# Kernel optimization log

Hardware: AMD Instinct MI355X
Metric: run time of the kernel (lower is better)

The kernel has to match this reference:

```python
import jax, jax.numpy as jnp
import numpy as np

B, S, F = 4, 8192, 32
D, H, L = 512, 8, 4
FD = 128
WIN = 256
CF = 4
MAXSEQ = 8192
HD = D // H
NEG = -1e9


def _ln(x, g, b, eps=1e-5):
    m = jnp.mean(x, -1, keepdims=True)
    v = jnp.var(x, -1, keepdims=True)
    return (x - m) * jax.lax.rsqrt(v + eps) * g + b


def setup_inputs() -> dict:
    key = jax.random.key(0)
    ks = iter(jax.random.split(key, 64))
    def rn(shape, s=0.02):
        return jax.random.normal(next(ks), shape, dtype=jnp.float32) * s
    return dict(
        x=jax.random.normal(next(ks), (B, S, F), dtype=jnp.float32),
        timestamps=jax.random.randint(next(ks), (B, S), 0, MAXSEQ),
        W_feat=rn((F, FD)), b_feat=jnp.zeros((FD,), jnp.float32),
        emb_temp=rn((MAXSEQ, FD)),
        W_emb=rn((2 * FD, D)), b_emb=jnp.zeros((D,), jnp.float32),
        Wq=rn((L, D, D)), bq=jnp.zeros((L, D), jnp.float32),
        Wk=rn((L, D, D)), bk=jnp.zeros((L, D), jnp.float32),
        Wv=rn((L, D, D)), bv=jnp.zeros((L, D), jnp.float32),
        Wo=rn((L, D, D)), bo=jnp.zeros((L, D), jnp.float32),
        Wg=rn((L, 2 * D, D)), bg=jnp.zeros((L, D), jnp.float32),
        Wu=rn((L, 2 * D, D)), bu=jnp.zeros((L, D), jnp.float32),
        ln_g=jnp.ones((L, D), jnp.float32), ln_b=jnp.zeros((L, D), jnp.float32),
        conv_w=rn((D, D, CF)), conv_b=jnp.zeros((D,), jnp.float32),
        cn_g=jnp.ones((D,), jnp.float32), cn_b=jnp.zeros((D,), jnp.float32),
        on_g=jnp.ones((D,), jnp.float32), on_b=jnp.zeros((D,), jnp.float32),
        W_out=rn((D, F)), b_out=jnp.zeros((F,), jnp.float32),
    )


def _sparse_attn(h, wq, bq, wk, bk, wv, bv, wo, bo):
    # sliding-window attention: query block b ([b*W,(b+1)*W)) attends keys in
    # [max(0,(b-1)*W), (b+1)*W) with plain softmax (no intra-window causal mask)
    bsz, slen, _ = h.shape
    nb = slen // WIN
    def proj(wm, bm):
        return (h @ wm + bm).reshape(bsz, nb, WIN, H, HD)
    q, k, v = proj(wq, bq), proj(wk, bk), proj(wv, bv)
    def with_prev(t):
        prev = jnp.concatenate([jnp.zeros_like(t[:, :1]), t[:, :-1]], axis=1)
        return jnp.concatenate([prev, t], axis=2)  # [B, nb, 2W, H, HD]
    kk, vv = with_prev(k), with_prev(v)
    scores = jnp.einsum('bnqhd,bnkhd->bnhqk', q, kk) / float(np.sqrt(HD))
    blk = jnp.arange(nb)[:, None]
    kidx = jnp.arange(2 * WIN)[None, :]
    neg = jnp.where((blk == 0) & (kidx < WIN), NEG, 0.0).astype(scores.dtype)
    att = jax.nn.softmax(scores + neg[None, :, None, None, :], axis=-1)
    out = jnp.einsum('bnhqk,bnkhd->bnqhd', att, vv).reshape(bsz, slen, D)
    return out @ wo + bo


def reference(x, timestamps, W_feat, b_feat, emb_temp, W_emb, b_emb,
              Wq, bq, Wk, bk, Wv, bv, Wo, bo, Wg, bg, Wu, bu,
              ln_g, ln_b, conv_w, conv_b, cn_g, cn_b, on_g, on_b, W_out, b_out):
    fe = x @ W_feat + b_feat                       # [B,S,FD]
    te = emb_temp[timestamps]                      # [B,S,FD]
    h = jnp.concatenate([fe, te], axis=-1) @ W_emb + b_emb  # [B,S,D]
    mem0 = jnp.zeros_like(h)

    def layer(carry, p):
        hh, mem = carry
        wq, bq_, wk, bk_, wv, bv_, wo, bo_, wg, bg_, wu, bu_, g, bta = p
        a = _sparse_attn(hh, wq, bq_, wk, bk_, wv, bv_, wo, bo_)
        comb = jnp.concatenate([a, mem], axis=-1)
        gate = jax.nn.sigmoid(comb @ wg + bg_)
        upd = comb @ wu + bu_
        new_mem = gate * upd + (1.0 - gate) * mem
        out = _ln(a + new_mem, g, bta)
        return (out, new_mem), None

    (h, _), _ = jax.lax.scan(
        layer, (h, mem0),
        (Wq, bq, Wk, bk, Wv, bv, Wo, bo, Wg, bg, Wu, bu, ln_g, ln_b))

    # temporal compression: Conv1d with kernel=stride=CF -> block reshape + einsum
    xr = h.reshape(h.shape[0], -1, CF, D)          # [B, S/CF, CF, D]
    c = jnp.einsum('btjc,ocj->bto', xr, conv_w) + conv_b
    c = _ln(c, cn_g, cn_b)
    o = _ln(c, on_g, on_b)
    return o @ W_out + b_out                       # [B, S/CF, F]
```

## Files before the change

kernel.cpp:

```cpp
#include <hip/hip_runtime.h>

#define BATCH   4
#define SEQ     8192
#define NTOK    32768
#define FF      32
#define FDIM    128
#define DD      512
#define HEADS   8
#define HDIM    64
#define WINSZ   256
#define NBLK    32
#define LAYERS  4

typedef unsigned short u16;
typedef __attribute__((ext_vector_type(8))) short bf16x8;
typedef __attribute__((ext_vector_type(4))) float f32x4;

__device__ __forceinline__ float u2f(u16 u) {
  return __uint_as_float(((unsigned int)u) << 16);
}
__device__ __forceinline__ u16 f2u(float f) {
  return (u16)((__float_as_uint(f) + 0x8000u) >> 16);
}
__device__ __forceinline__ unsigned int pk2(float a, float b) {
  return ((__float_as_uint(a) + 0x8000u) >> 16) |
         ((__float_as_uint(b) + 0x8000u) & 0xffff0000u);
}
__device__ __forceinline__ void ld8(const u16* __restrict__ p, float* o) {
  ushort4 q0 = *(const ushort4*)p;
  ushort4 q1 = *(const ushort4*)(p + 4);
  o[0]=u2f(q0.x); o[1]=u2f(q0.y); o[2]=u2f(q0.z); o[3]=u2f(q0.w);
  o[4]=u2f(q1.x); o[5]=u2f(q1.y); o[6]=u2f(q1.z); o[7]=u2f(q1.w);
}
__device__ __forceinline__ void st8(u16* __restrict__ p, const float* v) {
  uint4 o;
  o.x = pk2(v[0], v[1]); o.y = pk2(v[2], v[3]);
  o.z = pk2(v[4], v[5]); o.w = pk2(v[6], v[7]);
  *(uint4*)p = o;
}
__device__ __forceinline__ void gl_lds16(const u16* g, u16* l) {
  __builtin_amdgcn_global_load_lds(
      (const __attribute__((address_space(1))) void*)g,
      (__attribute__((address_space(3))) void*)l, 16, 0, 0);
}

__global__ __launch_bounds__(128) void embed_kernel(
    const float* __restrict__ x, const int* __restrict__ ts,
    const float* __restrict__ W_feat, const float* __restrict__ b_feat,
    const float* __restrict__ emb, u16* __restrict__ cat)
{
  const int t = blockIdx.x;
  const int j = threadIdx.x;
  __shared__ float xs[FF];
  if (j < FF) xs[j] = x[(size_t)t*FF + j];
  __syncthreads();
  float fe = b_feat[j];
  #pragma unroll
  for (int f = 0; f < FF; ++f) fe += xs[f] * W_feat[f*FDIM + j];
  cat[(size_t)t*256 + j] = f2u(fe);
  const int tv = ts[t];
  cat[(size_t)t*256 + 128 + j] = f2u(emb[(size_t)tv*FDIM + j]);
}

__global__ __launch_bounds__(256) void transpose_w(
    const float* __restrict__ src, u16* __restrict__ dst, int K)
{
  __shared__ u16 t[32][34];
  const int bk = blockIdx.x*32, bn = blockIdx.y*32;
  const int c = threadIdx.x & 31, r8 = threadIdx.x >> 5;
  #pragma unroll
  for (int rr = 0; rr < 32; rr += 8)
    t[rr + r8][c] = f2u(src[(size_t)(bk + rr + r8)*512 + bn + c]);
  __syncthreads();
  #pragma unroll
  for (int rr = 0; rr < 32; rr += 8)
    dst[(size_t)(bn + rr + r8)*K + bk + c] = t[c][rr + r8];
}

#define WQO 0
#define WKO 262144
#define WVO 524288
#define WOO 786432
#define WGO 1048576
#define WUO 1572864

__global__ __launch_bounds__(256) void convert_layer(
    const float* __restrict__ Wq, const float* __restrict__ Wk,
    const float* __restrict__ Wv, const float* __restrict__ Wo,
    const float* __restrict__ Wg, const float* __restrict__ Wu,
    u16* __restrict__ out)
{
  __shared__ u16 t[32][34];
  const int z = blockIdx.z;
  const int K = (z < 4) ? 512 : 1024;
  const int bk = blockIdx.x*32;
  if (bk >= K) return;
  const int bn = blockIdx.y*32;
  const float* src = (z==0)?Wq:(z==1)?Wk:(z==2)?Wv:(z==3)?Wo:(z==4)?Wg:Wu;
  u16* dst = out + ((z<4) ? (size_t)z*262144 : (size_t)1048576 + (size_t)(z-4)*524288);
  const int c = threadIdx.x & 31, r8 = threadIdx.x >> 5;
  #pragma unroll
  for (int rr = 0; rr < 32; rr += 8)
    t[rr + r8][c] = f2u(src[(size_t)(bk + rr + r8)*512 + bn + c]);
  __syncthreads();
  #pragma unroll
  for (int rr = 0; rr < 32; rr += 8)
    dst[(size_t)(bn + rr + r8)*K + bk + c] = t[c][rr + r8];
}

__global__ __launch_bounds__(256) void repack_conv(
    const float* __restrict__ cw, u16* __restrict__ dst)
{
  const int t = blockIdx.x*256 + threadIdx.x;
  const int o  = t >> 11;
  const int kk = t & 2047;
  const int j  = kk >> 9;
  const int ch = kk & 511;
  dst[t] = f2u(cw[(size_t)o*2048 + ch*4 + j]);
}

template<int MODE>
__global__ __launch_bounds__(512) void mfma_gemm(
    const u16* __restrict__ A1, const u16* __restrict__ A2, int K1, int K,
    const u16* __restrict__ Bt,
    const float* __restrict__ b0, const float* __restrict__ b1,
    const float* __restrict__ b2,
    u16* __restrict__ C0, u16* __restrict__ C1, u16* __restrict__ C2)
{
  __shared__ u16 Al[128*32];
  __shared__ u16 Bl[256*32];
  const int tid  = threadIdx.x;
  const int lane = tid & 63;
  const int wave = tid >> 6;
  const int wm = (wave & 1) * 64;
  const int wn = (wave >> 1) * 64;
  const int bid = blockIdx.x + gridDim.x * blockIdx.y;
  const int xcd = bid & 7;
  const int jj  = bid >> 3;
  const int nx  = jj % gridDim.x;
  const int my  = (jj / gridDim.x) * 8 + xcd;
  const int m0 = my * 128;
  const int n0 = nx * 256;
  const int cl = lane & 15, quad = lane >> 4;
  const int arow = tid >> 2;
  const int ak   = (tid & 3) * 8;
  u16* Adst  = Al + wave*512;
  u16* Bdst0 = Bl + wave*512;
  u16* Bdst1 = Bl + 4096 + wave*512;
  const int K2 = K - K1;

  f32x4 acc[4][4];
  #pragma unroll
  for (int i = 0; i < 4; ++i)
    #pragma unroll
    for (int j = 0; j < 4; ++j)
      acc[i][j] = (f32x4){0.f, 0.f, 0.f, 0.f};

  for (int k0 = 0; k0 < K; k0 += 32) {
    const int kc = k0 + ak;
    const u16* a = (kc < K1) ? A1 + (size_t)(m0 + arow)*K1 + kc
                             : A2 + (size_t)(m0 + arow)*K2 + (kc - K1);
    gl_lds16(a, Adst);
    gl_lds16(Bt + (size_t)(n0 + arow)*K + kc,       Bdst0);
    gl_lds16(Bt + (size_t)(n0 + 128 + arow)*K + kc, Bdst1);
    __syncthreads();
    bf16x8 af[4], bfr[4];
    #pragma unroll
    for (int i = 0; i < 4; ++i) {
      af[i]  = *(const bf16x8*)(Al + (wm + i*16 + cl)*32 + quad*8);
      bfr[i] = *(const bf16x8*)(Bl + (wn + i*16 + cl)*32 + quad*8);
    }
    #pragma unroll
    for (int i = 0; i < 4; ++i)
      #pragma unroll
      for (int j = 0; j < 4; ++j)
        acc[i][j] = __builtin_amdgcn_mfma_f32_16x16x32_bf16(
            af[i], bfr[j], acc[i][j], 0, 0, 0);
    __syncthreads();
  }
  const int rq = quad * 4;
  const int colbase = n0 + wn;
  const int seg = colbase >> 9;
  const float* bias = (MODE == 0) ? b0 : (seg == 0 ? b0 : (seg == 1 ? b1 : b2));
  u16* dstR = (seg == 0) ? C0 : C1;
  #pragma unroll
  for (int j = 0; j < 4; ++j) {
    const int lc = (colbase & 511) + j*16 + cl;
    const float bb = bias[lc];
    #pragma unroll
    for (int i = 0; i < 4; ++i) {
      const int rbase = m0 + wm + i*16 + rq;
      float v[4];
      #pragma unroll
      for (int r = 0; r < 4; ++r) {
        float t = acc[i][j][r] + bb;
        if (MODE == 2 && seg == 0) t = 1.0f / (1.0f + __expf(-t));
        v[r] = t;
      }
      if (MODE == 1 && seg == 2) {
        uint2 o2;
        o2.x = pk2(v[0], v[1]); o2.y = pk2(v[2], v[3]);
        *(uint2*)(C2 + (size_t)lc*NTOK + rbase) = o2;
      } else {
        #pragma unroll
        for (int r = 0; r < 4; ++r)
          dstR[(size_t)(rbase + r)*DD + lc] = f2u(v[r]);
      }
    }
  }
}

#define EXPSC 0.18033688f
__global__ __launch_bounds__(256) void attn_kernel(
    const u16* __restrict__ q, const u16* __restrict__ k,
    const u16* __restrict__ vt, u16* __restrict__ ctx)
{
  __shared__ u16 Ks[128*72];
  __shared__ u16 Vl[64*136];
  const int bid  = blockIdx.x;
  const int head = bid & 7;
  const int n    = (bid >> 3) & 31;
  const int b    = bid >> 8;
  const int tid  = threadIdx.x;
  const int lane = tid & 63;
  const int wave = tid >> 6;
  const int cl   = lane & 15;
  const int quad = lane >> 4;
  const int qtok0 = b*SEQ + n*WINSZ + wave*64;
  const bool hi2 = (lane >= 32);
  const int srcA = cl + ((quad & 1) << 5);
  const int srcB = srcA + 16;

  bf16x8 qf[4][2];
  #pragma unroll
  for (int jf = 0; jf < 4; ++jf)
    #pragma unroll
    for (int kh = 0; kh < 2; ++kh)
      qf[jf][kh] = *(const bf16x8*)(q + (size_t)(qtok0 + jf*16 + cl)*DD
                                      + head*HDIM + kh*32 + quad*8);

  f32x4 oacc[4][4];
  #pragma unroll
  for (int i = 0; i < 4; ++i)
    #pragma unroll
    for (int j = 0; j < 4; ++j)
      oacc[i][j] = (f32x4){0.f, 0.f, 0.f, 0.f};
  float lrun[4] = {0.f, 0.f, 0.f, 0.f};

  const int r0 = (n == 0) ? WINSZ : 0;
  const int base_tok = b*SEQ + (n - 1)*WINSZ;
  const int ksr = tid >> 1;
  const int ksc = (tid & 1) * 32;
  const int vsr = tid >> 2;
  const int vsc = (tid & 3) * 32;

  for (int c0 = r0; c0 < 2*WINSZ; c0 += 128) {
    {
      const u16* ksrc = k + (size_t)(base_tok + c0 + ksr)*DD + head*HDIM + ksc;
      uint4* kd = (uint4*)(Ks + ksr*72 + ksc);
      kd[0] = ((const uint4*)ksrc)[0];
      kd[1] = ((const uint4*)ksrc)[1];
      kd[2] = ((const uint4*)ksrc)[2];
      kd[3] = ((const uint4*)ksrc)[3];
      const u16* vsrc = vt + (size_t)(head*HDIM + vsr)*NTOK + base_tok + c0 + vsc;
      uint4* vd = (uint4*)(Vl + vsr*136 + vsc);
      vd[0] = ((const uint4*)vsrc)[0];
      vd[1] = ((const uint4*)vsrc)[1];
      vd[2] = ((const uint4*)vsrc)[2];
      vd[3] = ((const uint4*)vsrc)[3];
    }
    __syncthreads();
    #pragma unroll
    for (int half = 0; half < 2; ++half) {
      #pragma unroll
      for (int jf = 0; jf < 4; ++jf) {
        f32x4 sa[4];
        #pragma unroll
        for (int i = 0; i < 4; ++i) {
          const u16* kr = Ks + (half*64 + i*16 + cl)*72 + quad*8;
          bf16x8 k0 = *(const bf16x8*)kr;
          bf16x8 k1 = *(const bf16x8*)(kr + 32);
          f32x4 s = (f32x4){0.f, 0.f, 0.f, 0.f};
          s = __builtin_amdgcn_mfma_f32_16x16x32_bf16(k0, qf[jf][0], s, 0, 0, 0);
          s = __builtin_amdgcn_mfma_f32_16x16x32_bf16(k1, qf[jf][1], s, 0, 0, 0);
          sa[i] = s;
        }
        float rs = 0.f;
        unsigned int pd[4][2];
        #pragma unroll
        for (int i = 0; i < 4; ++i) {
          const float p0 = exp2f(sa[i][0] * EXPSC);
          const float p1 = exp2f(sa[i][1] * EXPSC);
          const float p2 = exp2f(sa[i][2] * EXPSC);
          const float p3 = exp2f(sa[i][3] * EXPSC);
          rs += (p0 + p1) + (p2 + p3);
          pd[i][0] = pk2(p0, p1);
          pd[i][1] = pk2(p2, p3);
        }
        rs += __shfl_xor(rs, 16, 64);
        rs += __shfl_xor(rs, 32, 64);
        lrun[jf] += rs;
        #pragma unroll
        for (int kh = 0; kh < 2; ++kh) {
          const int aA0 = __shfl((int)pd[2*kh][0],   srcA, 64);
          const int aB0 = __shfl((int)pd[2*kh+1][0], srcA, 64);
          const int aA1 = __shfl((int)pd[2*kh][1],   srcA, 64);
          const int aB1 = __shfl((int)pd[2*kh+1][1], srcA, 64);
          const int cA0 = __shfl((int)pd[2*kh][0],   srcB, 64);
          const int cB0 = __shfl((int)pd[2*kh+1][0], srcB, 64);
          const int cA1 = __shfl((int)pd[2*kh][1],   srcB, 64);
          const int cB1 = __shfl((int)pd[2*kh+1][1], srcB, 64);
          uint4 pw;
          pw.x = hi2 ? aB0 : aA0;
          pw.y = hi2 ? aB1 : aA1;
          pw.z = hi2 ? cB0 : cA0;
          pw.w = hi2 ? cB1 : cA1;
          bf16x8 pf = *(bf16x8*)&pw;
          #pragma unroll
          for (int jd = 0; jd < 4; ++jd) {
            bf16x8 vf = *(const bf16x8*)(Vl + (jd*16 + cl)*136
                                            + half*64 + kh*32 + quad*8);
            oacc[jd][jf] = __builtin_amdgcn_mfma_f32_16x16x32_bf16(
                vf, pf, oacc[jd][jf], 0, 0, 0);
          }
        }
      }
    }
    __syncthreads();
  }
  #pragma unroll
  for (int jq = 0; jq < 4; ++jq) {
    const float inv = 1.0f / lrun[jq];
    u16* crow = ctx + (size_t)(qtok0 + jq*16 + cl)*DD + head*HDIM + quad*4;
    #pragma unroll
    for (int jd = 0; jd < 4; ++jd) {
      uint2 o2;
      o2.x = pk2(oacc[jd][jq][0]*inv, oacc[jd][jq][1]*inv);
      o2.y = pk2(oacc[jd][jq][2]*inv, oacc[jd][jq][3]*inv);
      *(uint2*)(crow + jd*16) = o2;
    }
  }
}

__global__ __launch_bounds__(256) void memln_kernel(
    const u16* __restrict__ a, const u16* __restrict__ gate, const u16* __restrict__ upd,
    u16* __restrict__ mem, const float* __restrict__ lg, const float* __restrict__ lb,
    u16* __restrict__ h)
{
  const int lane = threadIdx.x & 63;
  const int wave = threadIdx.x >> 6;
  const int t = blockIdx.x*4 + wave;
  const size_t base = (size_t)t*DD + lane*8;
  float av[8], gv[8], uv[8], mv[8];
  ld8(a + base, av); ld8(gate + base, gv); ld8(upd + base, uv); ld8(mem + base, mv);
  float s[8], nm[8], sum = 0.f, sq = 0.f;
  #pragma unroll
  for (int e = 0; e < 8; ++e) {
    nm[e] = gv[e]*uv[e] + (1.0f - gv[e])*mv[e];
    s[e]  = av[e] + nm[e];
    sum  += s[e]; sq += s[e]*s[e];
  }
  st8(mem + base, nm);
  for (int o = 32; o > 0; o >>= 1) {
    sum += __shfl_xor(sum, o, 64);
    sq  += __shfl_xor(sq,  o, 64);
  }
  const float mean = sum * (1.0f/512.0f);
  const float var  = sq  * (1.0f/512.0f) - mean*mean;
  const float r = rsqrtf(var + 1e-5f);
  float y[8];
  #pragma unroll
  for (int e = 0; e < 8; ++e) {
    const int ch = lane*8 + e;
    y[e] = (s[e] - mean)*r*lg[ch] + lb[ch];
  }
  st8(h + base, y);
}

__global__ __launch_bounds__(256) void final_kernel(
    const u16* __restrict__ c,
    const float* __restrict__ cng, const float* __restrict__ cnb,
    const float* __restrict__ ong, const float* __restrict__ onb,
    const float* __restrict__ Wout, const float* __restrict__ bout,
    float* __restrict__ out)
{
  __shared__ float ybuf[4][512];
  const int lane = threadIdx.x & 63;
  const int wave = threadIdx.x >> 6;
  const int t = blockIdx.x*4 + wave;
  const size_t base = (size_t)t*DD + lane*8;
  float x[8];
  ld8(c + base, x);
  float sum = 0.f, sq = 0.f;
  #pragma unroll
  for (int e = 0; e < 8; ++e) { sum += x[e]; sq += x[e]*x[e]; }
  for (int o = 32; o > 0; o >>= 1) { sum += __shfl_xor(sum, o, 64); sq += __shfl_xor(sq, o, 64); }
  float mean = sum * (1.0f/512.0f);
  float var  = sq  * (1.0f/512.0f) - mean*mean;
  float r = rsqrtf(var + 1e-5f);
  float y[8];
  float sum2 = 0.f, sq2 = 0.f;
  #pragma unroll
  for (int e = 0; e < 8; ++e) {
    const int ch = lane*8 + e;
    y[e] = (x[e] - mean)*r*cng[ch] + cnb[ch];
    sum2 += y[e]; sq2 += y[e]*y[e];
  }
  for (int o = 32; o > 0; o >>= 1) { sum2 += __shfl_xor(sum2, o, 64); sq2 += __shfl_xor(sq2, o, 64); }
  mean = sum2 * (1.0f/512.0f);
  var  = sq2  * (1.0f/512.0f) - mean*mean;
  r = rsqrtf(var + 1e-5f);
  #pragma unroll
  for (int e = 0; e < 8; ++e) {
    const int ch = lane*8 + e;
    ybuf[wave][ch] = (y[e] - mean)*r*ong[ch] + onb[ch];
  }
  __syncthreads();
  if (lane < FF) {
    float acc = bout[lane];
    for (int ch = 0; ch < 512; ++ch)
      acc += ybuf[wave][ch] * Wout[ch*FF + lane];
    out[(size_t)t*FF + lane] = acc;
  }
}

extern "C" void kernel_launch(void* const* d_in, const int* in_sizes, int n_in,
                              void* d_out, int out_size, void* d_ws, size_t ws_size,
                              hipStream_t stream)
{
  const float* x      = (const float*)d_in[0];
  const int*   tstamp = (const int*)d_in[1];
  const float* W_feat = (const float*)d_in[2];
  const float* b_feat = (const float*)d_in[3];
  const float* emb_t  = (const float*)d_in[4];
  const float* W_emb  = (const float*)d_in[5];
  const float* b_emb  = (const float*)d_in[6];
  const float* Wq = (const float*)d_in[7];   const float* bq = (const float*)d_in[8];
  const float* Wk = (const float*)d_in[9];   const float* bk = (const float*)d_in[10];
  const float* Wv = (const float*)d_in[11];  const float* bv = (const float*)d_in[12];
  const float* Wo = (const float*)d_in[13];  const float* bo = (const float*)d_in[14];
  const float* Wg = (const float*)d_in[15];  const float* bg = (const float*)d_in[16];
  const float* Wu = (const float*)d_in[17];  const float* bu = (const float*)d_in[18];
  const float* lng = (const float*)d_in[19]; const float* lnb = (const float*)d_in[20];
  const float* convw = (const float*)d_in[21]; const float* convb = (const float*)d_in[22];
  const float* cng = (const float*)d_in[23]; const float* cnb = (const float*)d_in[24];
  const float* ong = (const float*)d_in[25]; const float* onb = (const float*)d_in[26];
  const float* Wout = (const float*)d_in[27]; const float* bout = (const float*)d_in[28];
  float* outp = (float*)d_out;

  char* ws = (char*)d_ws;
  const size_t MB = 1024u*1024u;
  u16* mem = (u16*)ws;
  u16* B1  = (u16*)(ws + 32*MB);
  u16* B2  = (u16*)(ws + 64*MB);
  u16* B3  = (u16*)(ws + 96*MB);
  u16* B4  = (u16*)(ws + 128*MB);
  u16* WB  = (u16*)(ws + 160*MB);

  hipMemsetAsync(mem, 0, (size_t)NTOK*DD*sizeof(u16), stream);

  embed_kernel<<<NTOK, 128, 0, stream>>>(x, tstamp, W_feat, b_feat, emb_t, B2);
  transpose_w<<<dim3(8, 16), 256, 0, stream>>>(W_emb, WB, 256);
  mfma_gemm<0><<<dim3(2, NTOK/128), 512, 0, stream>>>(
      B2, B2, 256, 256, WB, b_emb, nullptr, nullptr, B1, nullptr, nullptr);

  for (int l = 0; l < LAYERS; ++l) {
    convert_layer<<<dim3(32, 16, 6), 256, 0, stream>>>(
        Wq + (size_t)l*DD*DD, Wk + (size_t)l*DD*DD, Wv + (size_t)l*DD*DD,
        Wo + (size_t)l*DD*DD, Wg + (size_t)l*2*DD*DD, Wu + (size_t)l*2*DD*DD, WB);
    mfma_gemm<1><<<dim3(6, NTOK/128), 512, 0, stream>>>(
        B1, B1, 512, 512, WB + WQO,
        bq + l*DD, bk + l*DD, bv + l*DD, B2, B3, B4);
    attn_kernel<<<BATCH*NBLK*HEADS, 256, 0, stream>>>(B2, B3, B4, B1);
    mfma_gemm<0><<<dim3(2, NTOK/128), 512, 0, stream>>>(
        B1, B1, 512, 512, WB + WOO, bo + l*DD, nullptr, nullptr,
        B2, nullptr, nullptr);
    mfma_gemm<2><<<dim3(4, NTOK/128), 512, 0, stream>>>(
        B2, mem, 512, 1024, WB + WGO,
        bg + l*DD, bu + l*DD, nullptr, B3, B4, nullptr);
    memln_kernel<<<NTOK/4, 256, 0, stream>>>(
        B2, B3, B4, mem, lng + l*DD, lnb + l*DD, B1);
  }

  repack_conv<<<4096, 256, 0, stream>>>(convw, WB);
  mfma_gemm<0><<<dim3(2, 8192/128), 512, 0, stream>>>(
      B1, B1, 2048, 2048, WB, convb, nullptr, nullptr, B3, nullptr, nullptr);

  final_kernel<<<8192/4, 256, 0, stream>>>(
      B3, cng, cnb, ong, onb, Wout, bout, outp);
}
```

Measured before the change: 1.583 ms.

## Double GEMM K-step per barrier and split attention query blocks across two CTAs

The GEMM now loads two 32-wide K slices into separate LDS buffers per iteration, halving the number of barrier pairs and giving each wave more MFMA work between syncs. Attention grid doubles: each block handles 128 queries (32 per wave) instead of 256, raising occupancy and parallelism at the cost of reloading each K/V window twice. LDS use in the GEMM doubles, which may reduce occupancy.

```diff
diff --git a/kernel.cpp b/kernel.cpp
--- a/kernel.cpp
+++ b/kernel.cpp
@@ -127,8 +127,10 @@
     const float* __restrict__ b2,
     u16* __restrict__ C0, u16* __restrict__ C1, u16* __restrict__ C2)
 {
-  __shared__ u16 Al[128*32];
-  __shared__ u16 Bl[256*32];
+  __shared__ u16 Al0[128*32];
+  __shared__ u16 Al1[128*32];
+  __shared__ u16 Bl0[256*32];
+  __shared__ u16 Bl1[256*32];
   const int tid  = threadIdx.x;
   const int lane = tid & 63;
   const int wave = tid >> 6;
@@ -144,9 +146,12 @@
   const int cl = lane & 15, quad = lane >> 4;
   const int arow = tid >> 2;
   const int ak   = (tid & 3) * 8;
-  u16* Adst  = Al + wave*512;
-  u16* Bdst0 = Bl + wave*512;
-  u16* Bdst1 = Bl + 4096 + wave*512;
+  u16* Ad0 = Al0 + wave*512;
+  u16* Ad1 = Al1 + wave*512;
+  u16* Bd00 = Bl0 + wave*512;
+  u16* Bd01 = Bl0 + 4096 + wave*512;
+  u16* Bd10 = Bl1 + wave*512;
+  u16* Bd11 = Bl1 + 4096 + wave*512;
   const int K2 = K - K1;
 
   f32x4 acc[4][4];
@@ -156,26 +161,37 @@
     for (int j = 0; j < 4; ++j)
       acc[i][j] = (f32x4){0.f, 0.f, 0.f, 0.f};
 
-  for (int k0 = 0; k0 < K; k0 += 32) {
-    const int kc = k0 + ak;
-    const u16* a = (kc < K1) ? A1 + (size_t)(m0 + arow)*K1 + kc
-                             : A2 + (size_t)(m0 + arow)*K2 + (kc - K1);
-    gl_lds16(a, Adst);
-    gl_lds16(Bt + (size_t)(n0 + arow)*K + kc,       Bdst0);
-    gl_lds16(Bt + (size_t)(n0 + 128 + arow)*K + kc, Bdst1);
+  for (int k0 = 0; k0 < K; k0 += 64) {
+    const int kc0 = k0 + ak;
+    const int kc1 = kc0 + 32;
+    const u16* a0 = (kc0 < K1) ? A1 + (size_t)(m0 + arow)*K1 + kc0
+                               : A2 + (size_t)(m0 + arow)*K2 + (kc0 - K1);
+    const u16* a1 = (kc1 < K1) ? A1 + (size_t)(m0 + arow)*K1 + kc1
+                               : A2 + (size_t)(m0 + arow)*K2 + (kc1 - K1);
+    gl_lds16(a0, Ad0);
+    gl_lds16(a1, Ad1);
+    gl_lds16(Bt + (size_t)(n0 + arow)*K + kc0,       Bd00);
+    gl_lds16(Bt + (size_t)(n0 + 128 + arow)*K + kc0, Bd01);
+    gl_lds16(Bt + (size_t)(n0 + arow)*K + kc1,       Bd10);
+    gl_lds16(Bt + (size_t)(n0 + 128 + arow)*K + kc1, Bd11);
     __syncthreads();
-    bf16x8 af[4], bfr[4];
-    #pragma unroll
-    for (int i = 0; i < 4; ++i) {
-      af[i]  = *(const bf16x8*)(Al + (wm + i*16 + cl)*32 + quad*8);
-      bfr[i] = *(const bf16x8*)(Bl + (wn + i*16 + cl)*32 + quad*8);
+    #pragma unroll
+    for (int sub = 0; sub < 2; ++sub) {
+      const u16* Asrc = sub ? Al1 : Al0;
+      const u16* Bsrc = sub ? Bl1 : Bl0;
+      bf16x8 af[4], bfr[4];
+      #pragma unroll
+      for (int i = 0; i < 4; ++i) {
+        af[i]  = *(const bf16x8*)(Asrc + (wm + i*16 + cl)*32 + quad*8);
+        bfr[i] = *(const bf16x8*)(Bsrc + (wn + i*16 + cl)*32 + quad*8);
+      }
+      #pragma unroll
+      for (int i = 0; i < 4; ++i)
+        #pragma unroll
+        for (int j = 0; j < 4; ++j)
+          acc[i][j] = __builtin_amdgcn_mfma_f32_16x16x32_bf16(
+              af[i], bfr[j], acc[i][j], 0, 0, 0);
     }
-    #pragma unroll
-    for (int i = 0; i < 4; ++i)
-      #pragma unroll
-      for (int j = 0; j < 4; ++j)
-        acc[i][j] = __builtin_amdgcn_mfma_f32_16x16x32_bf16(
-            af[i], bfr[j], acc[i][j], 0, 0, 0);
     __syncthreads();
   }
   const int rq = quad * 4;
@@ -219,33 +235,34 @@
   __shared__ u16 Vl[64*136];
   const int bid  = blockIdx.x;
   const int head = bid & 7;
-  const int n    = (bid >> 3) & 31;
-  const int b    = bid >> 8;
+  const int qh   = (bid >> 3) & 1;
+  const int n    = (bid >> 4) & 31;
+  const int b    = bid >> 9;
   const int tid  = threadIdx.x;
   const int lane = tid & 63;
   const int wave = tid >> 6;
   const int cl   = lane & 15;
   const int quad = lane >> 4;
-  const int qtok0 = b*SEQ + n*WINSZ + wave*64;
+  const int qtok0 = b*SEQ + n*WINSZ + qh*128 + wave*32;
   const bool hi2 = (lane >= 32);
   const int srcA = cl + ((quad & 1) << 5);
   const int srcB = srcA + 16;
 
-  bf16x8 qf[4][2];
-  #pragma unroll
-  for (int jf = 0; jf < 4; ++jf)
+  bf16x8 qf[2][2];
+  #pragma unroll
+  for (int jf = 0; jf < 2; ++jf)
     #pragma unroll
     for (int kh = 0; kh < 2; ++kh)
       qf[jf][kh] = *(const bf16x8*)(q + (size_t)(qtok0 + jf*16 + cl)*DD
                                       + head*HDIM + kh*32 + quad*8);
 
-  f32x4 oacc[4][4];
+  f32x4 oacc[4][2];
   #pragma unroll
   for (int i = 0; i < 4; ++i)
     #pragma unroll
-    for (int j = 0; j < 4; ++j)
+    for (int j = 0; j < 2; ++j)
       oacc[i][j] = (f32x4){0.f, 0.f, 0.f, 0.f};
-  float lrun[4] = {0.f, 0.f, 0.f, 0.f};
+  float lrun[2] = {0.f, 0.f};
 
   const int r0 = (n == 0) ? WINSZ : 0;
   const int base_tok = b*SEQ + (n - 1)*WINSZ;
@@ -273,7 +290,7 @@
     #pragma unroll
     for (int half = 0; half < 2; ++half) {
       #pragma unroll
-      for (int jf = 0; jf < 4; ++jf) {
+      for (int jf = 0; jf < 2; ++jf) {
         f32x4 sa[4];
         #pragma unroll
         for (int i = 0; i < 4; ++i) {
@@ -329,7 +346,7 @@
     __syncthreads();
   }
   #pragma unroll
-  for (int jq = 0; jq < 4; ++jq) {
+  for (int jq = 0; jq < 2; ++jq) {
     const float inv = 1.0f / lrun[jq];
     u16* crow = ctx + (size_t)(qtok0 + jq*16 + cl)*DD + head*HDIM + quad*4;
     #pragma unroll
@@ -471,7 +488,7 @@
     mfma_gemm<1><<<dim3(6, NTOK/128), 512, 0, stream>>>(
         B1, B1, 512, 512, WB + WQO,
         bq + l*DD, bk + l*DD, bv + l*DD, B2, B3, B4);
-    attn_kernel<<<BATCH*NBLK*HEADS, 256, 0, stream>>>(B2, B3, B4, B1);
+    attn_kernel<<<BATCH*NBLK*2*HEADS, 256, 0, stream>>>(B2, B3, B4, B1);
     mfma_gemm<0><<<dim3(2, NTOK/128), 512, 0, stream>>>(
         B1, B1, 512, 512, WB + WOO, bo + l*DD, nullptr, nullptr,
         B2, nullptr, nullptr);
```

Result: faster. 1.422 ms (-10.1%).
